# Kernel optimization log

Measured on AMD Instinct MI355X. Metric: run time of the kernel, lower is better.

Reference implementation:

```python
import jax, jax.numpy as jnp
import numpy as np

K = 3          # kernel / stride
D = 32         # bond dimension
OUT = 10       # output classes
N_SITES = 27   # feature_dim after squeeze = C * k**3 = 27 -> sites per MPS


def squeeze_3d(img, k=K):
    # space-to-depth with channel sum, feature order (x,y,z) matching the
    # original nested-loop kernel extraction: feature = x*k*k + y*k + z
    H, V, Dd, C = img.shape
    x = img.reshape(H // k, k, V // k, k, Dd // k, k, C)
    x = x.transpose(0, 2, 4, 1, 3, 5, 6).sum(-1)  # (nH,nV,nD,k,k,k)
    return x.reshape(H // k, V // k, Dd // k, k ** 3)


def embed_trig(x):
    # trigonometric embedding, phys_dim = 2
    a = (jnp.pi / 2.0) * x
    return jnp.stack([jnp.cos(a), jnp.sin(a)], axis=-1)


def mps_chain(first, mid, last, e):
    # Batched tensor-train (SMPO with one output leg on site 0) contraction.
    # first: (N,2,O,D)   site 0, phys leg 2, output leg O, right bond D
    # mid:   (N,M,D,2,D) sites 1..n-2
    # last:  (N,D,2)     site n-1
    # e:     (N,n,2)     embedded inputs
    v0 = jnp.einsum('npod,np->nod', first, e[:, 0])              # (N,O,D)
    mats = jnp.einsum('nmdpe,nmp->nmde', mid, e[:, 1:-1])        # (N,M,D,D)

    def step(v, M):
        return jnp.einsum('nod,nde->noe', v, M), None

    v, _ = jax.lax.scan(step, v0, jnp.moveaxis(mats, 1, 0))
    return jnp.einsum('nod,ndp,np->no', v, last, e[:, -1])       # (N,O)


def unsqueeze_3d(v):
    # (N, feat) -> (s,s,s,1) with mean over feature dim
    n, f = v.shape
    s = round(n ** (1.0 / 3.0))
    return v.reshape(s, s, s, f).mean(-1, keepdims=True)


def setup_inputs():
    key = jax.random.key(0)
    ks = jax.random.split(key, 10)
    scale = 1.0 / np.sqrt(D)  # keeps 27-site matrix chain numerically stable
    mk = lambda k, sh: jax.random.normal(k, sh, dtype=jnp.float32) * scale
    n = N_SITES
    return {
        'input_image': jax.random.uniform(ks[0], (27, 27, 27, 1), dtype=jnp.float32),
        'l0_first': mk(ks[1], (729, 2, 1, D)),
        'l0_mid':   mk(ks[2], (729, n - 2, D, 2, D)),
        'l0_last':  mk(ks[3], (729, D, 2)),
        'l1_first': mk(ks[4], (27, 2, 1, D)),
        'l1_mid':   mk(ks[5], (27, n - 2, D, 2, D)),
        'l1_last':  mk(ks[6], (27, D, 2)),
        'f_first':  mk(ks[7], (2, OUT, D)),
        'f_mid':    mk(ks[8], (n - 2, D, 2, D)),
        'f_last':   mk(ks[9], (D, 2)),
    }


def reference(input_image, l0_first, l0_mid, l0_last,
              l1_first, l1_mid, l1_last, f_first, f_mid, f_last):
    # Layer 0: (27,27,27,1) -> squeeze (9,9,9,27) -> 729 MPS contractions
    sq = squeeze_3d(input_image).reshape(729, N_SITES)
    out0 = mps_chain(l0_first, l0_mid, l0_last, embed_trig(sq))   # (729,1)
    x = unsqueeze_3d(out0)                                        # (9,9,9,1)

    # Layer 1: (9,9,9,1) -> squeeze (3,3,3,27) -> 27 MPS contractions
    sq = squeeze_3d(x).reshape(27, N_SITES)
    out1 = mps_chain(l1_first, l1_mid, l1_last, embed_trig(sq))   # (27,1)
    x = unsqueeze_3d(out1)                                        # (3,3,3,1)

    # Final layer: (3,3,3,1) -> squeeze (1,1,1,27) -> one MPS with output leg
    sq = squeeze_3d(x).reshape(1, N_SITES)
    out = mps_chain(f_first[None], f_mid[None], f_last[None], embed_trig(sq))
    return out.reshape(OUT)
```

## Files before the change

### kernel.cpp

```cpp
#include <hip/hip_runtime.h>
#include <math.h>

#define NSITES 27
#define NMID   25
#define DD     32

#define LOADB(BUF, S)                                                   \
    {                                                                   \
        const float4* pm_ = m4 + (size_t)(S) * 512;                     \
        _Pragma("unroll")                                               \
        for (int k = 0; k < 8; ++k) BUF[k] = pm_[64 * k];               \
    }

#define COMPUTE(BUF, EI)                                                \
    {                                                                   \
        __syncthreads();                                                \
        const float e0_ = sE[EI][0];                                    \
        const float e1_ = sE[EI][1];                                    \
        float4 acc; acc.x = acc.y = acc.z = acc.w = 0.f;                \
        _Pragma("unroll")                                               \
        for (int k = 0; k < 8; ++k) {                                   \
            const float vd = sV[dbase + 4 * k];                         \
            acc.x = fmaf(BUF[k].x, vd, acc.x);                          \
            acc.y = fmaf(BUF[k].y, vd, acc.y);                          \
            acc.z = fmaf(BUF[k].z, vd, acc.z);                          \
            acc.w = fmaf(BUF[k].w, vd, acc.w);                          \
        }                                                               \
        _Pragma("unroll")                                               \
        for (int mask = 16; mask <= 32; mask <<= 1) {                   \
            acc.x += __shfl_xor(acc.x, mask, 64);                       \
            acc.y += __shfl_xor(acc.y, mask, 64);                       \
            acc.z += __shfl_xor(acc.z, mask, 64);                       \
            acc.w += __shfl_xor(acc.w, mask, 64);                       \
        }                                                               \
        float4 oth;                                                     \
        oth.x = __shfl_xor(acc.x, 8, 64);                               \
        oth.y = __shfl_xor(acc.y, 8, 64);                               \
        oth.z = __shfl_xor(acc.z, 8, 64);                               \
        oth.w = __shfl_xor(acc.w, 8, 64);                               \
        const float cm = p ? e1_ : e0_;                                 \
        const float co = p ? e0_ : e1_;                                 \
        float4 nv;                                                      \
        nv.x = fmaf(cm, acc.x, co * oth.x);                             \
        nv.y = fmaf(cm, acc.y, co * oth.y);                             \
        nv.z = fmaf(cm, acc.z, co * oth.z);                             \
        nv.w = fmaf(cm, acc.w, co * oth.w);                             \
        if (lane < 8) sV4[lane] = nv;                                   \
    }

__global__ __launch_bounds__(64) void mps_layer_kernel(
    const float* __restrict__ src,
    const float* __restrict__ first,
    const float* __restrict__ mid,
    const float* __restrict__ last,
    float*       __restrict__ out,
    int B, int nChains)
{
    const int lane = threadIdx.x;
    const int n = blockIdx.x;
    if (n >= nChains) return;

    __shared__ float  sE[NSITES][2];
    __shared__ float4 sV4[8];
    float* sV = (float*)sV4;

    const int S = 3 * B;
    const int bh = n / (B * B);
    const int bv = (n / B) % B;
    const int bd = n % B;

    if (lane < NSITES) {
        const int kh = lane / 9, kv = (lane / 3) % 3, kd = lane % 3;
        const float x = src[(size_t)(bh*3 + kh) * S * S + (bv*3 + kv) * S + (bd*3 + kd)];
        float sn, cs;
        sincosf(1.5707963267948966f * x, &sn, &cs);
        sE[lane][0] = cs;
        sE[lane][1] = sn;
    }
    __syncthreads();
    if (lane < DD) {
        const float* f = first + (size_t)n * (2 * DD);
        sV[lane] = fmaf(f[lane], sE[0][0], f[DD + lane] * sE[0][1]);
    }

    const int p     = (lane >> 3) & 1;
    const int dbase = lane >> 4;
    const float4* m4 = (const float4*)(mid + (size_t)n * NMID * 2048) + lane;

    float4 b0[8], b1[8], b2[8];
    LOADB(b0, 0)
    LOADB(b1, 1)
    LOADB(b2, 2)

    for (int m = 0; m < 24; m += 3) {
        COMPUTE(b0, m + 1)
        if (m + 3 < NMID) LOADB(b0, m + 3)
        COMPUTE(b1, m + 2)
        if (m + 4 < NMID) LOADB(b1, m + 4)
        COMPUTE(b2, m + 3)
        if (m + 5 < NMID) LOADB(b2, m + 5)
    }
    COMPUTE(b0, 25)
    __syncthreads();

    const float le0 = sE[26][0], le1 = sE[26][1];
    float tacc = 0.f;
    if (lane < DD) {
        const float* L = last + (size_t)n * (DD * 2);
        tacc = sV[lane] * fmaf(L[2 * lane], le0, L[2 * lane + 1] * le1);
    }
#pragma unroll
    for (int mask = 1; mask < 64; mask <<= 1) tacc += __shfl_xor(tacc, mask, 64);
    if (lane == 0) out[n] = tacc;
}

__global__ __launch_bounds__(64) void mps_final_kernel(
    const float* __restrict__ x,
    const float* __restrict__ ffirst,
    const float* __restrict__ fmid,
    const float* __restrict__ flast,
    float*       __restrict__ out)
{
    const int lane = threadIdx.x;
    __shared__ float sE[NSITES][2];
    __shared__ float sU[DD];

    if (lane < NSITES) {
        float sn, cs;
        sincosf(1.5707963267948966f * x[lane], &sn, &cs);
        sE[lane][0] = cs;
        sE[lane][1] = sn;
    }
    if (lane < DD) {
        sU[lane] = fmaf(flast[2 * lane], sE[26][0], flast[2 * lane + 1] * sE[26][1]);
    }

    const int p     = (lane >> 3) & 1;
    const int e4    = lane & 7;
    const int dbase = lane >> 4;
    const float4* m4 = (const float4*)fmid + lane;

    for (int m = NMID - 1; m >= 0; --m) {
        const float e0 = sE[m + 1][0];
        const float e1 = sE[m + 1][1];
        const float ep = p ? e1 : e0;
        const float4* mm = m4 + (size_t)m * 512;

        const float4 u4 = ((const float4*)sU)[e4];
        const float wx = ep * u4.x, wy = ep * u4.y, wz = ep * u4.z, ww = ep * u4.w;

        float acc[8];
#pragma unroll
        for (int k = 0; k < 8; ++k) {
            const float4 Mv = mm[64 * k];
            acc[k] = fmaf(Mv.x, wx, fmaf(Mv.y, wy, fmaf(Mv.z, wz, Mv.w * ww)));
        }
#pragma unroll
        for (int mask = 1; mask <= 8; mask <<= 1) {
#pragma unroll
            for (int k = 0; k < 8; ++k) acc[k] += __shfl_xor(acc[k], mask, 64);
        }
        if ((lane & 15) == 0) {
#pragma unroll
            for (int k = 0; k < 8; ++k) sU[dbase + 4 * k] = acc[k];
        }
    }

    const float e0 = sE[0][0], e1 = sE[0][1];
    const float ud = (lane < DD) ? sU[lane] : 0.f;
#pragma unroll
    for (int o = 0; o < 10; ++o) {
        float t = 0.f;
        if (lane < DD)
            t = fmaf(ffirst[o * DD + lane], e0, ffirst[320 + o * DD + lane] * e1) * ud;
#pragma unroll
        for (int mask = 1; mask < 64; mask <<= 1) t += __shfl_xor(t, mask, 64);
        if (lane == 0) out[o] = t;
    }
}

extern "C" void kernel_launch(void* const* d_in, const int* in_sizes, int n_in,
                              void* d_out, int out_size, void* d_ws, size_t ws_size,
                              hipStream_t stream) {
    const float* img = (const float*)d_in[0];
    const float* l0f = (const float*)d_in[1];
    const float* l0m = (const float*)d_in[2];
    const float* l0l = (const float*)d_in[3];
    const float* l1f = (const float*)d_in[4];
    const float* l1m = (const float*)d_in[5];
    const float* l1l = (const float*)d_in[6];
    const float* ff  = (const float*)d_in[7];
    const float* fm  = (const float*)d_in[8];
    const float* fl  = (const float*)d_in[9];
    float* out  = (float*)d_out;
    float* out0 = (float*)d_ws;
    float* out1 = out0 + 729;

    mps_layer_kernel<<<729, 64, 0, stream>>>(img,  l0f, l0m, l0l, out0, 9, 729);
    mps_layer_kernel<<<27,  64, 0, stream>>>(out0, l1f, l1m, l1l, out1, 3, 27);
    mps_final_kernel<<<1,   64, 0, stream>>>(out1, ff,  fm,  fl,  out);
}
```

Measured before the change: 278.2 us.

## Replace barriers with LDS waitcnt fences and pipeline final-layer matrix loads

Because each block is a single 64-lane wavefront, the per-site __syncthreads barriers are replaced with an s_waitcnt lgkmcnt(0) fence that only waits for outstanding LDS operations. The final single-chain kernel is restructured to prefetch site matrices into three register buffers, triple-buffered like the layer kernel, so global loads overlap with computation along the chain. This relies on the wavefront executing LDS writes and reads in program order. It also adds a fence in the final kernel that was previously missing between the sE writes and reads. The change risks compiler reordering across the inline asm and higher register pressure from the extra buffers.

```diff
diff --git a/kernel.cpp b/kernel.cpp
--- a/kernel.cpp
+++ b/kernel.cpp
@@ -5,6 +5,8 @@
 #define NMID   25
 #define DD     32
 
+#define FENCE asm volatile("s_waitcnt lgkmcnt(0)" ::: "memory");
+
 #define LOADB(BUF, S)                                                   \
     {                                                                   \
         const float4* pm_ = m4 + (size_t)(S) * 512;                     \
@@ -14,7 +16,7 @@
 
 #define COMPUTE(BUF, EI)                                                \
     {                                                                   \
-        __syncthreads();                                                \
+        FENCE                                                           \
         const float e0_ = sE[EI][0];                                    \
         const float e1_ = sE[EI][1];                                    \
         float4 acc; acc.x = acc.y = acc.z = acc.w = 0.f;                \
@@ -77,7 +79,7 @@
         sE[lane][0] = cs;
         sE[lane][1] = sn;
     }
-    __syncthreads();
+    FENCE
     if (lane < DD) {
         const float* f = first + (size_t)n * (2 * DD);
         sV[lane] = fmaf(f[lane], sE[0][0], f[DD + lane] * sE[0][1]);
@@ -101,7 +103,7 @@
         if (m + 5 < NMID) LOADB(b2, m + 5)
     }
     COMPUTE(b0, 25)
-    __syncthreads();
+    FENCE
 
     const float le0 = sE[26][0], le1 = sE[26][1];
     float tacc = 0.f;
@@ -113,6 +115,32 @@
     for (int mask = 1; mask < 64; mask <<= 1) tacc += __shfl_xor(tacc, mask, 64);
     if (lane == 0) out[n] = tacc;
 }
+
+#define FSITE(BUF, M)                                                   \
+    {                                                                   \
+        FENCE                                                           \
+        const float e0_ = sE[(M) + 1][0];                               \
+        const float e1_ = sE[(M) + 1][1];                               \
+        const float ep_ = p ? e1_ : e0_;                                \
+        const float4 u4 = ((const float4*)sU)[e4];                      \
+        const float wx = ep_ * u4.x, wy = ep_ * u4.y;                   \
+        const float wz = ep_ * u4.z, ww = ep_ * u4.w;                   \
+        float acc[8];                                                   \
+        _Pragma("unroll")                                               \
+        for (int k = 0; k < 8; ++k) {                                   \
+            const float4 Mv = BUF[k];                                   \
+            acc[k] = fmaf(Mv.x, wx, fmaf(Mv.y, wy, fmaf(Mv.z, wz, Mv.w * ww))); \
+        }                                                               \
+        _Pragma("unroll")                                               \
+        for (int mask = 1; mask <= 8; mask <<= 1) {                     \
+            _Pragma("unroll")                                           \
+            for (int k = 0; k < 8; ++k) acc[k] += __shfl_xor(acc[k], mask, 64); \
+        }                                                               \
+        if ((lane & 15) == 0) {                                         \
+            _Pragma("unroll")                                           \
+            for (int k = 0; k < 8; ++k) sU[dbase + 4 * k] = acc[k];     \
+        }                                                               \
+    }
 
 __global__ __launch_bounds__(64) void mps_final_kernel(
     const float* __restrict__ x,
@@ -131,6 +159,7 @@
         sE[lane][0] = cs;
         sE[lane][1] = sn;
     }
+    FENCE
     if (lane < DD) {
         sU[lane] = fmaf(flast[2 * lane], sE[26][0], flast[2 * lane + 1] * sE[26][1]);
     }
@@ -140,31 +169,22 @@
     const int dbase = lane >> 4;
     const float4* m4 = (const float4*)fmid + lane;
 
-    for (int m = NMID - 1; m >= 0; --m) {
-        const float e0 = sE[m + 1][0];
-        const float e1 = sE[m + 1][1];
-        const float ep = p ? e1 : e0;
-        const float4* mm = m4 + (size_t)m * 512;
-
-        const float4 u4 = ((const float4*)sU)[e4];
-        const float wx = ep * u4.x, wy = ep * u4.y, wz = ep * u4.z, ww = ep * u4.w;
-
-        float acc[8];
-#pragma unroll
-        for (int k = 0; k < 8; ++k) {
-            const float4 Mv = mm[64 * k];
-            acc[k] = fmaf(Mv.x, wx, fmaf(Mv.y, wy, fmaf(Mv.z, wz, Mv.w * ww)));
-        }
-#pragma unroll
-        for (int mask = 1; mask <= 8; mask <<= 1) {
-#pragma unroll
-            for (int k = 0; k < 8; ++k) acc[k] += __shfl_xor(acc[k], mask, 64);
-        }
-        if ((lane & 15) == 0) {
-#pragma unroll
-            for (int k = 0; k < 8; ++k) sU[dbase + 4 * k] = acc[k];
-        }
-    }
+    float4 c0[8], c1[8], c2[8];
+    LOADB(c0, 24)
+    LOADB(c1, 23)
+    LOADB(c2, 22)
+
+    for (int t = 0; t < 8; ++t) {
+        const int s0 = 24 - 3 * t;
+        FSITE(c0, s0)
+        if (s0 - 3 >= 0) LOADB(c0, s0 - 3)
+        FSITE(c1, s0 - 1)
+        if (s0 - 4 >= 0) LOADB(c1, s0 - 4)
+        FSITE(c2, s0 - 2)
+        if (s0 - 5 >= 0) LOADB(c2, s0 - 5)
+    }
+    FSITE(c0, 0)
+    FENCE
 
     const float e0 = sE[0][0], e1 = sE[0][1];
     const float ud = (lane < DD) ? sU[lane] : 0.f;
```

Result: faster. 270.1 us (-2.9%).
